# Performance work log

Measured on AMD Instinct MI355X. Metric: run time of the kernel, lower is better.

Reference implementation:

```python
import jax, jax.numpy as jnp
import numpy as np

N_NODES = 100000
N_EDGES = 1600000
F_IN, F_HID, F_OUT = 256, 128, 32


def setup_inputs() -> dict:
    key = jax.random.key(0)
    k1, k2, k3, k4 = jax.random.split(key, 4)
    x = jax.random.normal(k1, (N_NODES, F_IN), dtype=jnp.float32)
    edge_index = jax.random.randint(k2, (2, N_EDGES), 0, N_NODES, dtype=jnp.int64)
    W1 = jax.random.normal(k3, (F_IN, F_HID), dtype=jnp.float32) * (1.0 / np.sqrt(F_IN))
    b1 = jnp.zeros((F_HID,), dtype=jnp.float32)
    W2 = jax.random.normal(k4, (F_HID, F_OUT), dtype=jnp.float32) * (1.0 / np.sqrt(F_HID))
    b2 = jnp.zeros((F_OUT,), dtype=jnp.float32)
    return {"x": x, "edge_index": edge_index, "W1": W1, "b1": b1, "W2": W2, "b2": b2}


def _gcn_norm(edge_index, num_nodes):
    # Add self-loops, then symmetric normalization deg^-1/2[src] * deg^-1/2[dst].
    loops = jnp.arange(num_nodes, dtype=edge_index.dtype)
    src = jnp.concatenate([edge_index[0], loops])
    dst = jnp.concatenate([edge_index[1], loops])
    deg = jax.ops.segment_sum(jnp.ones_like(dst, dtype=jnp.float32), dst,
                              num_segments=num_nodes)
    dinv = jnp.where(deg > 0, jax.lax.rsqrt(deg), 0.0)
    norm = dinv[src] * dinv[dst]  # [E + N]
    return src, dst, norm


def _gcn_conv(h, src, dst, norm, num_nodes):
    # h already linearly transformed. Gather sources, scale, scatter-add to dst.
    msgs = h[src] * norm[:, None]
    return jax.ops.segment_sum(msgs, dst, num_segments=num_nodes)


def reference(x, edge_index, W1, b1, W2, b2):
    n = x.shape[0]
    src, dst, norm = _gcn_norm(edge_index, n)
    # Layer 1: linear -> normalized scatter-add -> bias -> relu
    h = _gcn_conv(x @ W1, src, dst, norm, n) + b1
    h = jax.nn.relu(h)
    # F.dropout with training=False (eval mode) is identity.
    # Layer 2
    out = _gcn_conv(h @ W2, src, dst, norm, n) + b2
    return jax.nn.log_softmax(out, axis=1)
```

## Files before the change

kernel.cpp:

```cpp
#include <hip/hip_runtime.h>

#define N_NODES 100000
#define N_EDGES 1600000
#define F_IN 256
#define F_HID 128
#define F_OUT 32
#define NBUCK 391
#define BIN_BLOCKS 512
#define EDGES_PER_BIN 3125
#define G1_BLOCKS 1563

typedef unsigned short ushort_t;
typedef unsigned int uint_t;

using short8  = __attribute__((ext_vector_type(8))) short;
using floatx4 = __attribute__((ext_vector_type(4))) float;

__device__ __forceinline__ ushort_t f2bf(float f) {
    uint_t u = __float_as_uint(f);
    u += 0x7fff + ((u >> 16) & 1);
    return (ushort_t)(u >> 16);
}
__device__ __forceinline__ float bf_lo(uint_t u) { return __uint_as_float(u << 16); }
__device__ __forceinline__ float bf_hi(uint_t u) { return __uint_as_float(u & 0xffff0000u); }
__device__ __forceinline__ uint_t bfpack_trunc(float a, float b) {
    return __builtin_amdgcn_perm(__float_as_uint(b), __float_as_uint(a), 0x07060302u);
}

__global__ __launch_bounds__(256) void histwt_kernel(const int* __restrict__ ei,
                                                     int* __restrict__ bucket_cnt,
                                                     const float* __restrict__ W1,
                                                     const float* __restrict__ W2,
                                                     ushort_t* __restrict__ W1T,
                                                     ushort_t* __restrict__ W2T) {
    __shared__ int h[NBUCK];
    if (blockIdx.x < BIN_BLOCKS) {
        for (int i = threadIdx.x; i < NBUCK; i += 256) h[i] = 0;
        __syncthreads();
        int gid = blockIdx.x * 256 + threadIdx.x;
        for (int e = gid; e < N_EDGES; e += BIN_BLOCKS * 256)
            atomicAdd(&h[ei[N_EDGES + e] >> 8], 1);
        __syncthreads();
        for (int i = threadIdx.x; i < NBUCK; i += 256) {
            int c = h[i];
            if (c) atomicAdd(&bucket_cnt[i], c);
        }
    } else {
        int t = (blockIdx.x - BIN_BLOCKS) * 256 + threadIdx.x;
#pragma unroll
        for (int j = 0; j < 4; j++) {
            int e = j * 8192 + t;
            int n = e >> 8, k = e & 255;
            W1T[e] = f2bf(W1[k * F_HID + n]);
        }
        if (t < 4096) {
            int n = t >> 7, k = t & 127;
            W2T[t] = f2bf(W2[k * F_OUT + n]);
        }
    }
}

__global__ __launch_bounds__(512) void scan_kernel(const int* __restrict__ bucket_cnt,
                                                   int* __restrict__ bucket_base,
                                                   int* __restrict__ bucket_cursor,
                                                   int* __restrict__ offs) {
    __shared__ int s[512];
    int t = threadIdx.x;
    int own = (t < NBUCK) ? bucket_cnt[t] : 0;
    s[t] = own;
    __syncthreads();
    for (int off = 1; off < 512; off <<= 1) {
        int v = (t >= off) ? s[t - off] : 0;
        __syncthreads();
        s[t] += v;
        __syncthreads();
    }
    if (t < NBUCK) {
        int ex = s[t] - own;
        bucket_base[t] = ex;
        bucket_cursor[t] = ex;
    }
    if (t == 0) {
        bucket_base[NBUCK] = N_EDGES;
        offs[N_NODES] = N_EDGES;
    }
}

__global__ __launch_bounds__(256) void bin_gemm1_kernel(const int* __restrict__ ei,
                                                        int* __restrict__ bucket_cursor,
                                                        int2* __restrict__ binned,
                                                        const float* __restrict__ x,
                                                        const ushort_t* __restrict__ W1T,
                                                        ushort_t* __restrict__ h0a,
                                                        ushort_t* __restrict__ h0b) {
    __shared__ __align__(16) char smem[(size_t)F_HID * (F_IN + 8) * 2];
    const int tid = threadIdx.x;
    if (blockIdx.x < BIN_BLOCKS) {
        int* h    = (int*)smem;
        int* base = ((int*)smem) + NBUCK;
        const int beg = blockIdx.x * EDGES_PER_BIN;
        const int end = beg + EDGES_PER_BIN;
        for (int i = tid; i < NBUCK; i += 256) h[i] = 0;
        __syncthreads();
        for (int e = beg + tid; e < end; e += 256) atomicAdd(&h[ei[N_EDGES + e] >> 8], 1);
        __syncthreads();
        for (int i = tid; i < NBUCK; i += 256) {
            int c = h[i];
            base[i] = c ? atomicAdd(&bucket_cursor[i], c) : 0;
            h[i] = 0;
        }
        __syncthreads();
        for (int e = beg + tid; e < end; e += 256) {
            int s = ei[e], d = ei[N_EDGES + e];
            int bk = d >> 8;
            int p = base[bk] + atomicAdd(&h[bk], 1);
            binned[p] = make_int2(s, d);
        }
    } else {
        ushort_t (*Bst)[F_IN + 8] = (ushort_t(*)[F_IN + 8])smem;
        const int rbase = (blockIdx.x - BIN_BLOCKS) * 64;
        const int w = tid >> 6;
        const int lane = tid & 63;
        const int q = lane >> 4;
        const int nloc = lane & 15;

#pragma unroll
        for (int j = 0; j < 16; j++) {
            int f = j * 256 + tid;
            int n = f >> 5, kg = f & 31;
            uint4 v = ((const uint4*)(W1T + n * F_IN))[kg];
            *(uint4*)(&Bst[n][kg * 8]) = v;
        }
        __syncthreads();

        const int rowA = rbase + w * 16 + nloc;
        const bool okA = rowA < N_NODES;
        const float* ap = x + (size_t)rowA * F_IN + q * 8;

        floatx4 acc[8];
#pragma unroll
        for (int t = 0; t < 8; t++) acc[t] = (floatx4){0.f, 0.f, 0.f, 0.f};

#pragma unroll
        for (int k0 = 0; k0 < F_IN; k0 += 32) {
            float4 f0 = make_float4(0.f, 0.f, 0.f, 0.f);
            float4 f1 = make_float4(0.f, 0.f, 0.f, 0.f);
            if (okA) {
                f0 = *(const float4*)(ap + k0);
                f1 = *(const float4*)(ap + k0 + 4);
            }
            uint4 au;
            au.x = bfpack_trunc(f0.x, f0.y);
            au.y = bfpack_trunc(f0.z, f0.w);
            au.z = bfpack_trunc(f1.x, f1.y);
            au.w = bfpack_trunc(f1.z, f1.w);
            short8 a = *(short8*)&au;
#pragma unroll
            for (int t = 0; t < 8; t++) {
                short8 b = *(const short8*)(&Bst[t * 16 + nloc][k0 + q * 8]);
                acc[t] = __builtin_amdgcn_mfma_f32_16x16x32_bf16(a, b, acc[t], 0, 0, 0);
            }
        }

#pragma unroll
        for (int reg = 0; reg < 4; reg++) {
            int rowD = rbase + w * 16 + q * 4 + reg;
            if (rowD < N_NODES) {
                ushort_t* opA = h0a + (size_t)rowD * 64 + nloc;
                ushort_t* opB = h0b + (size_t)rowD * 64 + nloc;
#pragma unroll
                for (int t = 0; t < 4; t++) opA[t * 16] = f2bf(acc[t][reg]);
#pragma unroll
                for (int t = 4; t < 8; t++) opB[(t - 4) * 16] = f2bf(acc[t][reg]);
            }
        }
    }
}

__global__ __launch_bounds__(256) void build_kernel(const int2* __restrict__ binned,
                                                    const int* __restrict__ bucket_base,
                                                    int* __restrict__ offs,
                                                    int* __restrict__ csr,
                                                    float* __restrict__ dinv,
                                                    int* __restrict__ degarr) {
    __shared__ int h[256];
    __shared__ int sc[256];
    __shared__ int cur[256];
    const int b = blockIdx.x, t = threadIdx.x;
    const int beg = bucket_base[b];
    const int end = bucket_base[b + 1];
    h[t] = 0;
    __syncthreads();
    for (int j = beg + t; j < end; j += 256) {
        int2 p = binned[j];
        atomicAdd(&h[p.y & 255], 1);
    }
    __syncthreads();
    int deg = h[t];
    sc[t] = deg;
    __syncthreads();
    for (int off = 1; off < 256; off <<= 1) {
        int v = (t >= off) ? sc[t - off] : 0;
        __syncthreads();
        sc[t] += v;
        __syncthreads();
    }
    int excl = sc[t] - deg;
    cur[t] = excl;
    int node = b * 256 + t;
    if (node < N_NODES) {
        offs[node] = beg + excl;
        dinv[node] = rsqrtf((float)deg + 1.0f);
        degarr[node] = deg;
    }
    __syncthreads();
    for (int j = beg + t; j < end; j += 256) {
        int2 p = binned[j];
        int pos = atomicAdd(&cur[p.y & 255], 1);
        csr[beg + pos] = p.x;
    }
}

__global__ __launch_bounds__(256) void pack_kernel(int* __restrict__ csr,
                                                   const int* __restrict__ degarr) {
    int i = blockIdx.x * 256 + threadIdx.x;
    if (i >= N_EDGES / 4) return;
    int4 c = ((int4*)csr)[i];
    c.x |= degarr[c.x] << 20;
    c.y |= degarr[c.y] << 20;
    c.z |= degarr[c.z] << 20;
    c.w |= degarr[c.w] << 20;
    ((int4*)csr)[i] = c;
}

__global__ __launch_bounds__(256) void gather64(const ushort_t* __restrict__ h0a,
                                                const ushort_t* __restrict__ h0b,
                                                const int* __restrict__ offs,
                                                const int* __restrict__ csr,
                                                const float* __restrict__ dinv,
                                                ushort_t* __restrict__ aggA,
                                                ushort_t* __restrict__ aggB) {
    const int half = blockIdx.x >= (N_NODES / 8);
    const int nb = blockIdx.x - half * (N_NODES / 8);
    const ushort_t* tab = half ? h0b : h0a;
    ushort_t* outt = half ? aggB : aggA;

    const int node = nb * 8 + (threadIdx.x >> 5);
    const int l = threadIdx.x & 31;
    const int sub = l >> 3;
    const int fl = l & 7;
    const float dn = dinv[node];
    const uint4* rowbase = (const uint4*)tab;

    uint4 sv = rowbase[(size_t)node * 8 + fl];
    float s = (sub == 0) ? dn * dn : 0.f;
    float a[8];
    a[0] = bf_lo(sv.x) * s; a[1] = bf_hi(sv.x) * s;
    a[2] = bf_lo(sv.y) * s; a[3] = bf_hi(sv.y) * s;
    a[4] = bf_lo(sv.z) * s; a[5] = bf_hi(sv.z) * s;
    a[6] = bf_lo(sv.w) * s; a[7] = bf_hi(sv.w) * s;

    const int beg = offs[node], end = offs[node + 1];
    for (int j = beg; j < end; j += 16) {
        uint_t w[4];
        float nn[4];
        uint4 r[4];
#pragma unroll
        for (int k = 0; k < 4; k++) w[k] = ((const uint_t*)csr)[j + 4 * k + sub];
#pragma unroll
        for (int k = 0; k < 4; k++) {
            bool v = (j + 4 * k + sub) < end;
            int src = v ? (int)(w[k] & 0xFFFFFu) : 0;
            nn[k] = v ? rsqrtf((float)(w[k] >> 20) + 1.0f) * dn : 0.f;
            r[k] = rowbase[(size_t)src * 8 + fl];
        }
#pragma unroll
        for (int k = 0; k < 4; k++) {
            float n = nn[k];
            a[0] += bf_lo(r[k].x) * n; a[1] += bf_hi(r[k].x) * n;
            a[2] += bf_lo(r[k].y) * n; a[3] += bf_hi(r[k].y) * n;
            a[4] += bf_lo(r[k].z) * n; a[5] += bf_hi(r[k].z) * n;
            a[6] += bf_lo(r[k].w) * n; a[7] += bf_hi(r[k].w) * n;
        }
    }
#pragma unroll
    for (int i = 0; i < 8; i++) {
        a[i] += __shfl_xor(a[i], 8);
        a[i] += __shfl_xor(a[i], 16);
    }
    if (sub == 0) {
        uint4 p;
        p.x = (uint_t)f2bf(a[0]) | ((uint_t)f2bf(a[1]) << 16);
        p.y = (uint_t)f2bf(a[2]) | ((uint_t)f2bf(a[3]) << 16);
        p.z = (uint_t)f2bf(a[4]) | ((uint_t)f2bf(a[5]) << 16);
        p.w = (uint_t)f2bf(a[6]) | ((uint_t)f2bf(a[7]) << 16);
        ((uint4*)outt)[(size_t)node * 8 + fl] = p;
    }
}

__global__ __launch_bounds__(256) void gemm2_kernel(const ushort_t* __restrict__ aggA,
                                                    const ushort_t* __restrict__ aggB,
                                                    const float* __restrict__ b1,
                                                    const ushort_t* __restrict__ W2T,
                                                    ushort_t* __restrict__ h2bf) {
    __shared__ ushort_t Bs[F_OUT][F_HID + 8];
    __shared__ float b1s[F_HID];
    const int tid = threadIdx.x;
    const int rbase = blockIdx.x * 64;
    const int w = tid >> 6;
    const int lane = tid & 63;
    const int q = lane >> 4;
    const int nloc = lane & 15;

    if (tid < F_HID) b1s[tid] = b1[tid];
#pragma unroll
    for (int jj = 0; jj < 2; jj++) {
        int f = jj * 256 + tid;
        int n = f >> 4, kg = f & 15;
        uint4 v = ((const uint4*)(W2T + n * F_HID))[kg];
        *(uint4*)(&Bs[n][kg * 8]) = v;
    }
    __syncthreads();

    const int rowA = rbase + w * 16 + nloc;
    const bool okA = rowA < N_NODES;

    floatx4 acc[2];
    acc[0] = (floatx4){0.f, 0.f, 0.f, 0.f};
    acc[1] = (floatx4){0.f, 0.f, 0.f, 0.f};

#pragma unroll
    for (int k0 = 0; k0 < F_HID; k0 += 32) {
        int kk = k0 + q * 8;
        const ushort_t* at = (k0 < 64) ? aggA : aggB;
        int kloc = (k0 < 64) ? kk : kk - 64;
        uint4 av = make_uint4(0, 0, 0, 0);
        if (okA) av = *(const uint4*)(at + (size_t)rowA * 64 + kloc);
        float4 bb0 = *(const float4*)(&b1s[kk]);
        float4 bb1 = *(const float4*)(&b1s[kk + 4]);
        uint4 au;
        au.x = bfpack_trunc(fmaxf(bf_lo(av.x) + bb0.x, 0.f), fmaxf(bf_hi(av.x) + bb0.y, 0.f));
        au.y = bfpack_trunc(fmaxf(bf_lo(av.y) + bb0.z, 0.f), fmaxf(bf_hi(av.y) + bb0.w, 0.f));
        au.z = bfpack_trunc(fmaxf(bf_lo(av.z) + bb1.x, 0.f), fmaxf(bf_hi(av.z) + bb1.y, 0.f));
        au.w = bfpack_trunc(fmaxf(bf_lo(av.w) + bb1.z, 0.f), fmaxf(bf_hi(av.w) + bb1.w, 0.f));
        short8 a = *(short8*)&au;
#pragma unroll
        for (int t = 0; t < 2; t++) {
            short8 b = *(const short8*)(&Bs[t * 16 + nloc][kk]);
            acc[t] = __builtin_amdgcn_mfma_f32_16x16x32_bf16(a, b, acc[t], 0, 0, 0);
        }
    }
#pragma unroll
    for (int reg = 0; reg < 4; reg++) {
        int rowD = rbase + w * 16 + q * 4 + reg;
        if (rowD < N_NODES) {
            ushort_t* op = h2bf + (size_t)rowD * F_OUT + nloc;
            op[0]  = f2bf(acc[0][reg]);
            op[16] = f2bf(acc[1][reg]);
        }
    }
}

__global__ __launch_bounds__(256) void gather32_lsm(const ushort_t* __restrict__ h2bf,
                                                    const int* __restrict__ offs,
                                                    const int* __restrict__ csr,
                                                    const float* __restrict__ dinv,
                                                    const float* __restrict__ b2,
                                                    float* __restrict__ out) {
    const int node = blockIdx.x * 8 + (threadIdx.x >> 5);
    const int l = threadIdx.x & 31;
    const int sub = l >> 2;
    const int fl = l & 3;
    const float dn = dinv[node];
    const uint4* rowbase = (const uint4*)h2bf;

    uint4 sv = rowbase[(size_t)node * 4 + fl];
    float s = (sub == 0) ? dn * dn : 0.f;
    float a[8];
    a[0] = bf_lo(sv.x) * s; a[1] = bf_hi(sv.x) * s;
    a[2] = bf_lo(sv.y) * s; a[3] = bf_hi(sv.y) * s;
    a[4] = bf_lo(sv.z) * s; a[5] = bf_hi(sv.z) * s;
    a[6] = bf_lo(sv.w) * s; a[7] = bf_hi(sv.w) * s;

    const int beg = offs[node], end = offs[node + 1];
    for (int j = beg; j < end; j += 16) {
        uint_t w[2];
        float nn[2];
        uint4 r[2];
#pragma unroll
        for (int k = 0; k < 2; k++) w[k] = ((const uint_t*)csr)[j + 8 * k + sub];
#pragma unroll
        for (int k = 0; k < 2; k++) {
            bool v = (j + 8 * k + sub) < end;
            int src = v ? (int)(w[k] & 0xFFFFFu) : 0;
            nn[k] = v ? rsqrtf((float)(w[k] >> 20) + 1.0f) * dn : 0.f;
            r[k] = rowbase[(size_t)src * 4 + fl];
        }
#pragma unroll
        for (int k = 0; k < 2; k++) {
            float n = nn[k];
            a[0] += bf_lo(r[k].x) * n; a[1] += bf_hi(r[k].x) * n;
            a[2] += bf_lo(r[k].y) * n; a[3] += bf_hi(r[k].y) * n;
            a[4] += bf_lo(r[k].z) * n; a[5] += bf_hi(r[k].z) * n;
            a[6] += bf_lo(r[k].w) * n; a[7] += bf_hi(r[k].w) * n;
        }
    }
#pragma unroll
    for (int i = 0; i < 8; i++) {
        a[i] += __shfl_xor(a[i], 4);
        a[i] += __shfl_xor(a[i], 8);
        a[i] += __shfl_xor(a[i], 16);
    }
    float4 bb0 = ((const float4*)b2)[fl * 2];
    float4 bb1 = ((const float4*)b2)[fl * 2 + 1];
    a[0] += bb0.x; a[1] += bb0.y; a[2] += bb0.z; a[3] += bb0.w;
    a[4] += bb1.x; a[5] += bb1.y; a[6] += bb1.z; a[7] += bb1.w;

    float m = a[0];
#pragma unroll
    for (int i = 1; i < 8; i++) m = fmaxf(m, a[i]);
    m = fmaxf(m, __shfl_xor(m, 1));
    m = fmaxf(m, __shfl_xor(m, 2));
    float es = 0.f;
#pragma unroll
    for (int i = 0; i < 8; i++) es += __expf(a[i] - m);
    es += __shfl_xor(es, 1);
    es += __shfl_xor(es, 2);
    float lse = m + __logf(es);

    if (sub == 0) {
        float4 o0 = make_float4(a[0] - lse, a[1] - lse, a[2] - lse, a[3] - lse);
        float4 o1 = make_float4(a[4] - lse, a[5] - lse, a[6] - lse, a[7] - lse);
        float4* op = (float4*)(out + (size_t)node * F_OUT);
        op[fl * 2] = o0;
        op[fl * 2 + 1] = o1;
    }
}

extern "C" void kernel_launch(void* const* d_in, const int* in_sizes, int n_in,
                              void* d_out, int out_size, void* d_ws, size_t ws_size,
                              hipStream_t stream) {
    const float* x  = (const float*)d_in[0];
    const int*   ei = (const int*)d_in[1];
    const float* W1 = (const float*)d_in[2];
    const float* b1 = (const float*)d_in[3];
    const float* W2 = (const float*)d_in[4];
    const float* b2 = (const float*)d_in[5];
    float* out = (float*)d_out;

    float* ws = (float*)d_ws;
    float*    dinv          = ws;
    int*      offs          = (int*)(ws + 100096);
    int*      bucket_cnt    = (int*)(ws + 200224);
    int*      bucket_base   = (int*)(ws + 200736);
    int*      bucket_cursor = (int*)(ws + 201248);
    int*      degarr        = (int*)(ws + 201760);
    int*      csr           = (int*)(ws + 301856);
    ushort_t* W1T           = (ushort_t*)(ws + 1901856);
    ushort_t* W2T           = (ushort_t*)(ws + 1918240);
    ushort_t* h0a           = (ushort_t*)(ws + 1920288);
    ushort_t* h0b           = (ushort_t*)(ws + 5120288);
    ushort_t* aggA          = (ushort_t*)(ws + 8320288);
    ushort_t* aggB          = (ushort_t*)(ws + 11520288);
    ushort_t* h2bf          = (ushort_t*)(ws + 14720288);
    int2*     binned        = (int2*)aggA;

    hipMemsetAsync(bucket_cnt, 0, 512 * sizeof(int), stream);
    histwt_kernel<<<BIN_BLOCKS + 32, 256, 0, stream>>>(ei, bucket_cnt, W1, W2, W1T, W2T);
    scan_kernel<<<1, 512, 0, stream>>>(bucket_cnt, bucket_base, bucket_cursor, offs);
    bin_gemm1_kernel<<<BIN_BLOCKS + G1_BLOCKS, 256, 0, stream>>>(ei, bucket_cursor, binned,
                                                                 x, W1T, h0a, h0b);
    build_kernel<<<NBUCK, 256, 0, stream>>>(binned, bucket_base, offs, csr, dinv, degarr);
    pack_kernel<<<(N_EDGES / 4 + 255) / 256, 256, 0, stream>>>(csr, degarr);
    gather64<<<2 * (N_NODES / 8), 256, 0, stream>>>(h0a, h0b, offs, csr, dinv, aggA, aggB);
    gemm2_kernel<<<(N_NODES + 63) / 64, 256, 0, stream>>>(aggA, aggB, b1, W2T, h2bf);
    gather32_lsm<<<N_NODES / 8, 256, 0, stream>>>(h2bf, offs, csr, dinv, b2, out);
}
```

Measured before the change: 339.9 us.

## Compute per-node degree up front, fold pack into build, chunk W1 LDS staging

The histogram pass now counts in-degree per node with global atomics, and a new small reduction kernel sums those counts into bucket counts. Because degrees are known before build, build can pack the source degree into each CSR entry directly, so the separate pack kernel goes away. The GEMM1 path stages W1 in LDS in four 64-wide K chunks instead of the full 256, which cuts shared memory per block to raise occupancy. In exchange it adds a 400KB memset, 1.6M global atomics spread over 100k addresses instead of LDS atomics, and extra barriers in the GEMM loop.

Result: slower. 383.6 us (+12.9%).

```diff
diff --git a/kernel.cpp b/kernel.cpp
--- a/kernel.cpp
+++ b/kernel.cpp
@@ -28,23 +28,15 @@
 }
 
 __global__ __launch_bounds__(256) void histwt_kernel(const int* __restrict__ ei,
-                                                     int* __restrict__ bucket_cnt,
+                                                     int* __restrict__ deg,
                                                      const float* __restrict__ W1,
                                                      const float* __restrict__ W2,
                                                      ushort_t* __restrict__ W1T,
                                                      ushort_t* __restrict__ W2T) {
-    __shared__ int h[NBUCK];
     if (blockIdx.x < BIN_BLOCKS) {
-        for (int i = threadIdx.x; i < NBUCK; i += 256) h[i] = 0;
-        __syncthreads();
         int gid = blockIdx.x * 256 + threadIdx.x;
         for (int e = gid; e < N_EDGES; e += BIN_BLOCKS * 256)
-            atomicAdd(&h[ei[N_EDGES + e] >> 8], 1);
-        __syncthreads();
-        for (int i = threadIdx.x; i < NBUCK; i += 256) {
-            int c = h[i];
-            if (c) atomicAdd(&bucket_cnt[i], c);
-        }
+            atomicAdd(&deg[ei[N_EDGES + e]], 1);
     } else {
         int t = (blockIdx.x - BIN_BLOCKS) * 256 + threadIdx.x;
 #pragma unroll
@@ -58,6 +50,19 @@
             W2T[t] = f2bf(W2[k * F_OUT + n]);
         }
     }
+}
+
+__global__ __launch_bounds__(256) void sum_kernel(const int* __restrict__ deg,
+                                                  int* __restrict__ bucket_cnt) {
+    __shared__ int red[4];
+    const int t = threadIdx.x;
+    int node = blockIdx.x * 256 + t;
+    int v = (node < N_NODES) ? deg[node] : 0;
+#pragma unroll
+    for (int off = 32; off; off >>= 1) v += __shfl_down(v, off);
+    if ((t & 63) == 0) red[t >> 6] = v;
+    __syncthreads();
+    if (t == 0) bucket_cnt[blockIdx.x] = red[0] + red[1] + red[2] + red[3];
 }
 
 __global__ __launch_bounds__(512) void scan_kernel(const int* __restrict__ bucket_cnt,
@@ -93,7 +98,7 @@
                                                         const ushort_t* __restrict__ W1T,
                                                         ushort_t* __restrict__ h0a,
                                                         ushort_t* __restrict__ h0b) {
-    __shared__ __align__(16) char smem[(size_t)F_HID * (F_IN + 8) * 2];
+    __shared__ __align__(16) char smem[(size_t)F_HID * 72 * 2];
     const int tid = threadIdx.x;
     if (blockIdx.x < BIN_BLOCKS) {
         int* h    = (int*)smem;
@@ -117,22 +122,13 @@
             binned[p] = make_int2(s, d);
         }
     } else {
-        ushort_t (*Bst)[F_IN + 8] = (ushort_t(*)[F_IN + 8])smem;
+        ushort_t (*Bst)[72] = (ushort_t(*)[72])smem;
         const int rbase = (blockIdx.x - BIN_BLOCKS) * 64;
         const int w = tid >> 6;
         const int lane = tid & 63;
         const int q = lane >> 4;
         const int nloc = lane & 15;
 
-#pragma unroll
-        for (int j = 0; j < 16; j++) {
-            int f = j * 256 + tid;
-            int n = f >> 5, kg = f & 31;
-            uint4 v = ((const uint4*)(W1T + n * F_IN))[kg];
-            *(uint4*)(&Bst[n][kg * 8]) = v;
-        }
-        __syncthreads();
-
         const int rowA = rbase + w * 16 + nloc;
         const bool okA = rowA < N_NODES;
         const float* ap = x + (size_t)rowA * F_IN + q * 8;
@@ -142,24 +138,37 @@
         for (int t = 0; t < 8; t++) acc[t] = (floatx4){0.f, 0.f, 0.f, 0.f};
 
 #pragma unroll
-        for (int k0 = 0; k0 < F_IN; k0 += 32) {
-            float4 f0 = make_float4(0.f, 0.f, 0.f, 0.f);
-            float4 f1 = make_float4(0.f, 0.f, 0.f, 0.f);
-            if (okA) {
-                f0 = *(const float4*)(ap + k0);
-                f1 = *(const float4*)(ap + k0 + 4);
+        for (int Q = 0; Q < 4; Q++) {
+#pragma unroll
+            for (int j = 0; j < 4; j++) {
+                int f = j * 256 + tid;
+                int n = f >> 3, kg = f & 7;
+                uint4 v = ((const uint4*)(W1T + n * F_IN + Q * 64))[kg];
+                *(uint4*)(&Bst[n][kg * 8]) = v;
             }
-            uint4 au;
-            au.x = bfpack_trunc(f0.x, f0.y);
-            au.y = bfpack_trunc(f0.z, f0.w);
-            au.z = bfpack_trunc(f1.x, f1.y);
-            au.w = bfpack_trunc(f1.z, f1.w);
-            short8 a = *(short8*)&au;
-#pragma unroll
-            for (int t = 0; t < 8; t++) {
-                short8 b = *(const short8*)(&Bst[t * 16 + nloc][k0 + q * 8]);
-                acc[t] = __builtin_amdgcn_mfma_f32_16x16x32_bf16(a, b, acc[t], 0, 0, 0);
+            __syncthreads();
+
+#pragma unroll
+            for (int k0 = 0; k0 < 64; k0 += 32) {
+                float4 f0 = make_float4(0.f, 0.f, 0.f, 0.f);
+                float4 f1 = make_float4(0.f, 0.f, 0.f, 0.f);
+                if (okA) {
+                    f0 = *(const float4*)(ap + Q * 64 + k0);
+                    f1 = *(const float4*)(ap + Q * 64 + k0 + 4);
+                }
+                uint4 au;
+                au.x = bfpack_trunc(f0.x, f0.y);
+                au.y = bfpack_trunc(f0.z, f0.w);
+                au.z = bfpack_trunc(f1.x, f1.y);
+                au.w = bfpack_trunc(f1.z, f1.w);
+                short8 a = *(short8*)&au;
+#pragma unroll
+                for (int t = 0; t < 8; t++) {
+                    short8 b = *(const short8*)(&Bst[t * 16 + nloc][k0 + q * 8]);
+                    acc[t] = __builtin_amdgcn_mfma_f32_16x16x32_bf16(a, b, acc[t], 0, 0, 0);
+                }
             }
+            __syncthreads();
         }
 
 #pragma unroll
@@ -179,10 +188,10 @@
 
 __global__ __launch_bounds__(256) void build_kernel(const int2* __restrict__ binned,
                                                     const int* __restrict__ bucket_base,
+                                                    const int* __restrict__ deg,
                                                     int* __restrict__ offs,
                                                     int* __restrict__ csr,
-                                                    float* __restrict__ dinv,
-                                                    int* __restrict__ degarr) {
+                                                    float* __restrict__ dinv) {
     __shared__ int h[256];
     __shared__ int sc[256];
     __shared__ int cur[256];
@@ -196,8 +205,8 @@
         atomicAdd(&h[p.y & 255], 1);
     }
     __syncthreads();
-    int deg = h[t];
-    sc[t] = deg;
+    int d = h[t];
+    sc[t] = d;
     __syncthreads();
     for (int off = 1; off < 256; off <<= 1) {
         int v = (t >= off) ? sc[t - off] : 0;
@@ -205,32 +214,19 @@
         sc[t] += v;
         __syncthreads();
     }
-    int excl = sc[t] - deg;
+    int excl = sc[t] - d;
     cur[t] = excl;
     int node = b * 256 + t;
     if (node < N_NODES) {
         offs[node] = beg + excl;
-        dinv[node] = rsqrtf((float)deg + 1.0f);
-        degarr[node] = deg;
+        dinv[node] = rsqrtf((float)d + 1.0f);
     }
     __syncthreads();
     for (int j = beg + t; j < end; j += 256) {
         int2 p = binned[j];
         int pos = atomicAdd(&cur[p.y & 255], 1);
-        csr[beg + pos] = p.x;
-    }
-}
-
-__global__ __launch_bounds__(256) void pack_kernel(int* __restrict__ csr,
-                                                   const int* __restrict__ degarr) {
-    int i = blockIdx.x * 256 + threadIdx.x;
-    if (i >= N_EDGES / 4) return;
-    int4 c = ((int4*)csr)[i];
-    c.x |= degarr[c.x] << 20;
-    c.y |= degarr[c.y] << 20;
-    c.z |= degarr[c.z] << 20;
-    c.w |= degarr[c.w] << 20;
-    ((int4*)csr)[i] = c;
+        csr[beg + pos] = p.x | (deg[p.x] << 20);
+    }
 }
 
 __global__ __launch_bounds__(256) void gather64(const ushort_t* __restrict__ h0a,
@@ -451,10 +447,10 @@
     float* ws = (float*)d_ws;
     float*    dinv          = ws;
     int*      offs          = (int*)(ws + 100096);
-    int*      bucket_cnt    = (int*)(ws + 200224);
-    int*      bucket_base   = (int*)(ws + 200736);
-    int*      bucket_cursor = (int*)(ws + 201248);
-    int*      degarr        = (int*)(ws + 201760);
+    int*      degarr        = (int*)(ws + 200224);
+    int*      bucket_cnt    = (int*)(ws + 300320);
+    int*      bucket_base   = (int*)(ws + 300832);
+    int*      bucket_cursor = (int*)(ws + 301344);
     int*      csr           = (int*)(ws + 301856);
     ushort_t* W1T           = (ushort_t*)(ws + 1901856);
     ushort_t* W2T           = (ushort_t*)(ws + 1918240);
@@ -465,13 +461,13 @@
     ushort_t* h2bf          = (ushort_t*)(ws + 14720288);
     int2*     binned        = (int2*)aggA;
 
-    hipMemsetAsync(bucket_cnt, 0, 512 * sizeof(int), stream);
-    histwt_kernel<<<BIN_BLOCKS + 32, 256, 0, stream>>>(ei, bucket_cnt, W1, W2, W1T, W2T);
+    hipMemsetAsync(degarr, 0, 100096 * sizeof(int), stream);
+    histwt_kernel<<<BIN_BLOCKS + 32, 256, 0, stream>>>(ei, degarr, W1, W2, W1T, W2T);
+    sum_kernel<<<NBUCK, 256, 0, stream>>>(degarr, bucket_cnt);
     scan_kernel<<<1, 512, 0, stream>>>(bucket_cnt, bucket_base, bucket_cursor, offs);
     bin_gemm1_kernel<<<BIN_BLOCKS + G1_BLOCKS, 256, 0, stream>>>(ei, bucket_cursor, binned,
                                                                  x, W1T, h0a, h0b);
-    build_kernel<<<NBUCK, 256, 0, stream>>>(binned, bucket_base, offs, csr, dinv, degarr);
-    pack_kernel<<<(N_EDGES / 4 + 255) / 256, 256, 0, stream>>>(csr, degarr);
+    build_kernel<<<NBUCK, 256, 0, stream>>>(binned, bucket_base, degarr, offs, csr, dinv);
     gather64<<<2 * (N_NODES / 8), 256, 0, stream>>>(h0a, h0b, offs, csr, dinv, aggA, aggB);
     gemm2_kernel<<<(N_NODES + 63) / 64, 256, 0, stream>>>(aggA, aggB, b1, W2T, h2bf);
     gather32_lsm<<<N_NODES / 8, 256, 0, stream>>>(h2bf, offs, csr, dinv, b2, out);
```
